# Kernel tuning notes

Hardware: AMD Instinct MI355X
Metric: run time of the kernel (lower is better)

## Reference

```python
import jax, jax.numpy as jnp
import numpy as np

B, E, FC_N = 8, 65536, 2500
CONVS = [5, 16, 32, 64, 64]
EPS = 1e-5


def setup_inputs() -> dict:
    key = jax.random.key(0)
    ks = iter(jax.random.split(key, 32))
    inp = {
        'x': jax.random.normal(next(ks), (B, 5, E), dtype=jnp.float32),
        'gemm': jax.random.randint(next(ks), (B, E, 4), 0, E, dtype=jnp.int32),
        'old_verts': jax.random.normal(next(ks), (B, 642, 3), dtype=jnp.float32),
    }
    for i in range(4):
        ci, co = CONVS[i], CONVS[i + 1]
        inp[f'w{i}'] = jax.random.normal(next(ks), (co, ci, 5), dtype=jnp.float32) * 0.02
        inp[f'b{i}'] = jnp.zeros((co,), dtype=jnp.float32)
        inp[f'g{i}'] = jnp.ones((co,), dtype=jnp.float32)
        inp[f'beta{i}'] = jnp.zeros((co,), dtype=jnp.float32)
    inp['dw1'] = jax.random.normal(next(ks), (FC_N, CONVS[-1]), dtype=jnp.float32) * 0.02
    inp['db1'] = jnp.zeros((FC_N,), dtype=jnp.float32)
    inp['dw2'] = jax.random.normal(next(ks), (642 * 3, FC_N), dtype=jnp.float32) * 0.02
    inp['db2'] = jnp.zeros((642 * 3,), dtype=jnp.float32)
    return inp


def mesh_conv(x, gemm, w, b):
    # x: (B,C,E); gemm: (B,E,4) -> neighbor features (B,C,E,4)
    nb = jax.vmap(lambda xb, gb: xb[:, gb])(x, gemm)
    # MeshCNN symmetric features: [self, a+c, b+d, |a-c|, |b-d|]
    f = jnp.stack([
        x,
        nb[..., 0] + nb[..., 2],
        nb[..., 1] + nb[..., 3],
        jnp.abs(nb[..., 0] - nb[..., 2]),
        jnp.abs(nb[..., 1] - nb[..., 3]),
    ], axis=-1)  # (B,C,E,5)
    return jnp.einsum('bcek,ock->boe', f, w) + b[None, :, None]


def bn_relu(x, g, beta):
    # BatchNorm2d training-mode math over (batch, spatial) per channel
    mean = jnp.mean(x, axis=(0, 2), keepdims=True)
    var = jnp.var(x, axis=(0, 2), keepdims=True)
    return jax.nn.relu((x - mean) * jax.lax.rsqrt(var + EPS) * g[None, :, None] + beta[None, :, None])


def reference(x, gemm, old_verts,
              w0, b0, g0, beta0, w1, b1, g1, beta1,
              w2, b2, g2, beta2, w3, b3, g3, beta3,
              dw1, db1, dw2, db2):
    h = x[:, :5]
    params = [(w0, b0, g0, beta0), (w1, b1, g1, beta1),
              (w2, b2, g2, beta2), (w3, b3, g3, beta3)]
    for w, b, g, beta in params:
        h = bn_relu(mesh_conv(h, gemm, w, b), g, beta)
    pooled = jnp.mean(h, axis=2)                 # AvgPool1d(n_edges) -> (B, C)
    h1 = jax.nn.relu(pooled @ dw1.T + db1)       # dropout = identity (eval)
    out = h1 @ dw2.T + db2
    return out.reshape(-1, 642, 3) + old_verts
```

## Files before the change

kernel.cpp:

```cpp
#include <hip/hip_runtime.h>

#define E_DIM 65536
#define BE_TOTAL 524288
#define EPS_BN 1e-5f
#define NB_STATS 256

typedef unsigned int uint;
typedef unsigned short ushort;
typedef unsigned char uchar;
typedef __attribute__((ext_vector_type(8))) short short8;
typedef __attribute__((ext_vector_type(4))) float floatx4;

#define PB_FP8 ((size_t)BE_TOTAL*16)

__device__ __forceinline__ float bflo(uint u){ return __uint_as_float(u << 16); }
__device__ __forceinline__ float bfhi(uint u){ return __uint_as_float(u & 0xffff0000u); }

__device__ __forceinline__ ushort pbf1(float a){
  uint ua = __float_as_uint(a);
  return (ushort)((ua + 0x7fffu + ((ua >> 16) & 1u)) >> 16);
}
__device__ __forceinline__ uint packbf(float a, float b){
  return (uint)pbf1(a) | ((uint)pbf1(b) << 16);
}
__device__ __forceinline__ void unpack8(uint4 v, float* x){
  x[0]=bflo(v.x); x[1]=bfhi(v.x); x[2]=bflo(v.y); x[3]=bfhi(v.y);
  x[4]=bflo(v.z); x[5]=bfhi(v.z); x[6]=bflo(v.w); x[7]=bfhi(v.w);
}
__device__ __forceinline__ uint4 pack8u(const float* z){
  uint4 v;
  v.x = packbf(z[0],z[1]); v.y = packbf(z[2],z[3]);
  v.z = packbf(z[4],z[5]); v.w = packbf(z[6],z[7]);
  return v;
}

__device__ __forceinline__ uint2 pack8f8(const float* z){
  int lo = __builtin_amdgcn_cvt_pk_fp8_f32(z[0], z[1], 0,  false);
  lo     = __builtin_amdgcn_cvt_pk_fp8_f32(z[2], z[3], lo, true);
  int hi = __builtin_amdgcn_cvt_pk_fp8_f32(z[4], z[5], 0,  false);
  hi     = __builtin_amdgcn_cvt_pk_fp8_f32(z[6], z[7], hi, true);
  uint2 r; r.x = (uint)lo; r.y = (uint)hi; return r;
}
__device__ __forceinline__ void dec8f8(uint2 w, float* x){
  x[0]=__builtin_amdgcn_cvt_f32_fp8((int)w.x,0);
  x[1]=__builtin_amdgcn_cvt_f32_fp8((int)w.x,1);
  x[2]=__builtin_amdgcn_cvt_f32_fp8((int)w.x,2);
  x[3]=__builtin_amdgcn_cvt_f32_fp8((int)w.x,3);
  x[4]=__builtin_amdgcn_cvt_f32_fp8((int)w.y,0);
  x[5]=__builtin_amdgcn_cvt_f32_fp8((int)w.y,1);
  x[6]=__builtin_amdgcn_cvt_f32_fp8((int)w.y,2);
  x[7]=__builtin_amdgcn_cvt_f32_fp8((int)w.y,3);
}
__device__ __forceinline__ uchar f8byte(float v){
  return (uchar)(__builtin_amdgcn_cvt_pk_fp8_f32(v, 0.f, 0, false) & 0xff);
}

template<int CI, int CO>
__global__ void wprep8(const float* __restrict__ w, uchar* __restrict__ img)
{
  constexpr int CHUNKS = CI/16;
  const int t = blockIdx.x*256 + threadIdx.x;
  if (t >= CHUNKS*3*CO*4) return;
  const int g  = t & 3;
  const int o  = (t >> 2) % CO;
  const int ck = (t >> 2) / CO;
  const int chunk = ck / 3;
  const int ks    = ck % 3;
  float z[8];
  #pragma unroll
  for (int j8=0;j8<8;j8++){
    const int j = g*8 + j8;
    const int ft = ks*2 + (j>>4);
    const int ci = chunk*16 + (j & 15);
    z[j8] = (ft < 5) ? w[((size_t)o*CI + ci)*5 + ft] * 64.f : 0.f;
  }
  const int t4 = (o&3) ^ ((o>>2)&3);
  *reinterpret_cast<uint2*>(img + ((size_t)(ck*CO + o))*32 + ((g^t4)<<3)) = pack8f8(z);
}

template<int CI, int CO, bool IN_FP8, bool OUT_BF16LIN>
__launch_bounds__(256, 4)
__global__ void mconv_mfma(const char* __restrict__ hin,
                           const int* __restrict__ gemm,
                           const char* __restrict__ wimg,
                           const float* __restrict__ bias, float bscale,
                           const float* __restrict__ ss, float pkf,
                           char* __restrict__ hout,
                           float* __restrict__ spart)
{
  constexpr int CHUNKS = CI/16;
  constexpr int NT = CO/16;
  constexpr int AB  = IN_FP8 ? 32 : 64;
  constexpr int FBY = 3*128*AB;
  constexpr int NBUF = (CHUNKS > 1) ? 2 : 1;
  constexpr int OBB = 128*CO*(OUT_BF16LIN?2:1);
  constexpr int SBY = 4*2*CO*4;
  constexpr int SMEM = (NBUF*FBY > OBB+SBY) ? NBUF*FBY : (OBB+SBY);
  constexpr size_t PIN = IN_FP8 ? PB_FP8 : (size_t)BE_TOTAL*32;
  constexpr int RB = IN_FP8 ? 16 : 32;
  __shared__ char smem[SMEM];
  char* FB = smem;

  const int tid = threadIdx.x;
  const int bid = blockIdx.x;
  const int b   = bid & 7;
  const int e0  = (bid >> 3) * 128;
  const size_t bbase = (size_t)b << 16;

  const int lane = tid & 63;
  const int wv   = tid >> 6;
  const int col  = lane & 15;
  const int kg   = lane >> 4;
  const int t4c  = (col & 3) ^ ((col >> 2) & 3);

  floatx4 acc[2][NT];
  #pragma unroll
  for (int n=0;n<NT;n++){
    const float bv = bias[n*16 + col] * bscale;
    #pragma unroll
    for (int mt=0;mt<2;mt++) acc[mt][n] = (floatx4){bv,bv,bv,bv};
  }

  const int el = tid >> 1;
  const int hh = tid & 1;
  const int t4e = (el&3) ^ ((el>>2)&3);
  uint off[5];
  {
    const size_t idx = bbase + (size_t)(e0 + el);
    const int4 g4 = *reinterpret_cast<const int4*>(gemm + idx*4);
    off[0] = (uint)(idx*RB + hh*(RB/2));
    off[1] = (uint)((bbase + (size_t)(uint)g4.x)*RB + hh*(RB/2));
    off[2] = (uint)((bbase + (size_t)(uint)g4.y)*RB + hh*(RB/2));
    off[3] = (uint)((bbase + (size_t)(uint)g4.z)*RB + hh*(RB/2));
    off[4] = (uint)((bbase + (size_t)(uint)g4.w)*RB + hh*(RB/2));
  }

  auto BUILD = [&](float (&v)[5][8], int chunk, char* FBb){
    const int cb = chunk*16 + hh*8;
    #pragma unroll
    for (int c=0;c<8;c++){
      const float sc = ss[cb+c], sh = ss[CI+cb+c];
      #pragma unroll
      for (int r=0;r<5;r++) v[r][c] = fmaxf(fmaf(v[r][c], sc, sh), 0.f);
    }
    float y[5][8];
    #pragma unroll
    for (int c=0;c<8;c++){
      y[0][c] = v[0][c];
      y[1][c] = v[1][c] + v[3][c];
      y[2][c] = v[2][c] + v[4][c];
      y[3][c] = fabsf(v[1][c] - v[3][c]);
      y[4][c] = fabsf(v[2][c] - v[4][c]);
    }
    if constexpr (IN_FP8){
      #pragma unroll
      for (int ks=0; ks<3; ks++){
        char* base = FBb + ks*(128*32) + el*32;
        *reinterpret_cast<uint2*>(base + (((0+hh)^t4e)<<3)) = pack8f8(y[2*ks]);
        if (ks < 2){
          *reinterpret_cast<uint2*>(base + (((2+hh)^t4e)<<3)) = pack8f8(y[2*ks+1]);
        } else {
          uint2 zz; zz.x=0u; zz.y=0u;
          *reinterpret_cast<uint2*>(base + (((2+hh)^t4e)<<3)) = zz;
        }
      }
    } else {
      #pragma unroll
      for (int ks=0; ks<3; ks++){
        char* base = FBb + ks*8192 + el*64;
        *reinterpret_cast<uint4*>(base + (((0+hh)^t4e)<<4)) = pack8u(y[2*ks]);
        if (ks < 2){
          *reinterpret_cast<uint4*>(base + (((2+hh)^t4e)<<4)) = pack8u(y[2*ks+1]);
        } else {
          const uint4 zz = {0,0,0,0};
          *reinterpret_cast<uint4*>(base + (((2+hh)^t4e)<<4)) = zz;
        }
      }
    }
  };

  auto MMA = [&](int chunk, const char* FBb){
    const char* WG = wimg + (size_t)chunk*(3*CO*AB);
    #pragma unroll
    for (int ks=0; ks<3; ks++){
      if constexpr (IN_FP8){
        long long bf[NT];
        #pragma unroll
        for (int n=0;n<NT;n++)
          bf[n] = *reinterpret_cast<const long long*>(WG + ks*(CO*32) + n*512 + col*32 + ((kg^t4c)<<3));
        #pragma unroll
        for (int mt=0;mt<2;mt++){
          const long long af = *reinterpret_cast<const long long*>(
              FBb + ks*(128*32) + (wv*32+mt*16+col)*32 + ((kg^t4c)<<3));
          #pragma unroll
          for (int n=0;n<NT;n++)
            acc[mt][n] = __builtin_amdgcn_mfma_f32_16x16x32_fp8_fp8(af, bf[n], acc[mt][n], 0, 0, 0);
        }
      } else {
        short8 bf[NT];
        #pragma unroll
        for (int n=0;n<NT;n++)
          bf[n] = *reinterpret_cast<const short8*>(WG + ks*(CO*64) + n*1024 + col*64 + ((kg^t4c)<<4));
        #pragma unroll
        for (int mt=0;mt<2;mt++){
          const short8 af = *reinterpret_cast<const short8*>(
              FBb + ks*8192 + (wv*32+mt*16+col)*64 + ((kg^t4c)<<4));
          #pragma unroll
          for (int n=0;n<NT;n++)
            acc[mt][n] = __builtin_amdgcn_mfma_f32_16x16x32_bf16(af, bf[n], acc[mt][n], 0, 0, 0);
        }
      }
    }
  };

  if constexpr (CHUNKS == 1){
    float v[5][8];
    uint2 q[5];
    #pragma unroll
    for (int r=0;r<5;r++) q[r] = *reinterpret_cast<const uint2*>(hin + off[r]);
    #pragma unroll
    for (int r=0;r<5;r++) dec8f8(q[r], v[r]);
    BUILD(v, 0, FB);
    __syncthreads();
    MMA(0, FB);
  } else {
    uint2 qs[2][5];
    #pragma unroll
    for (int r=0;r<5;r++) qs[0][r] = *reinterpret_cast<const uint2*>(hin + off[r]);
    {
      const char* hp1 = hin + PIN;
      #pragma unroll
      for (int r=0;r<5;r++) qs[1][r] = *reinterpret_cast<const uint2*>(hp1 + off[r]);
    }
    {
      float v[5][8];
      #pragma unroll
      for (int r=0;r<5;r++) dec8f8(qs[0][r], v[r]);
      BUILD(v, 0, FB);
    }
    __syncthreads();
    #pragma unroll
    for (int c=0; c<CHUNKS; ++c){
      if (c+2 < CHUNKS){
        const char* hp = hin + (size_t)(c+2)*PIN;
        #pragma unroll
        for (int r=0;r<5;r++) qs[c&1][r] = *reinterpret_cast<const uint2*>(hp + off[r]);
      }
      MMA(c, FB + (c&1)*FBY);
      if (c+1 < CHUNKS){
        float v[5][8];
        #pragma unroll
        for (int r=0;r<5;r++) dec8f8(qs[(c+1)&1][r], v[r]);
        BUILD(v, c+1, FB + ((c+1)&1)*FBY);
        __syncthreads();
      }
    }
  }

  float sred[2*NT];
  #pragma unroll
  for (int n=0;n<NT;n++){
    float s = 0.f, q2 = 0.f;
    #pragma unroll
    for (int mt=0;mt<2;mt++){
      #pragma unroll
      for (int r=0;r<4;r++){ const float vv = acc[mt][n][r]; s += vv; q2 = fmaf(vv,vv,q2); }
    }
    s  += __shfl_xor(s,16,64);  s  += __shfl_xor(s,32,64);
    q2 += __shfl_xor(q2,16,64); q2 += __shfl_xor(q2,32,64);
    sred[n] = s; sred[NT+n] = q2;
  }

  __syncthreads();
  float* SB = reinterpret_cast<float*>(smem + OBB);
  if constexpr (OUT_BF16LIN){
    ushort* OB = reinterpret_cast<ushort*>(smem);
    #pragma unroll
    for (int mt=0; mt<2; mt++){
      const int er = wv*32 + mt*16 + 4*kg;
      #pragma unroll
      for (int n=0;n<NT;n++){
        #pragma unroll
        for (int r=0;r<4;r++)
          OB[(er+r)*CO + n*16 + col] = pbf1(acc[mt][n][r]);
      }
    }
  } else {
    uchar* OB = reinterpret_cast<uchar*>(smem);
    #pragma unroll
    for (int mt=0; mt<2; mt++){
      const int er = wv*32 + mt*16 + 4*kg;
      #pragma unroll
      for (int n=0;n<NT;n++){
        #pragma unroll
        for (int r=0;r<4;r++)
          OB[(er+r)*CO + n*16 + col] = f8byte(acc[mt][n][r] * pkf);
      }
    }
  }
  if (kg == 0){
    #pragma unroll
    for (int n=0;n<NT;n++){
      SB[wv*2*CO + n*16 + col]      = sred[n];
      SB[wv*2*CO + CO + n*16 + col] = sred[NT+n];
    }
  }
  __syncthreads();
  if constexpr (OUT_BF16LIN){
    const uint4* src = reinterpret_cast<const uint4*>(smem);
    uint4* dst = reinterpret_cast<uint4*>(hout + (bbase + (size_t)e0)*CO*2);
    constexpr int NV = 128*CO/8;
    for (int i=tid; i<NV; i+=256) dst[i] = src[i];
  } else {
    constexpr int NV = 128*CO/16;
    for (int i=tid; i<NV; i+=256){
      const int pl  = i >> 7;
      const int elx = i & 127;
      const uint4 vv = *reinterpret_cast<const uint4*>(smem + elx*CO + pl*16);
      *reinterpret_cast<uint4*>(hout + (size_t)pl*PB_FP8 + (bbase + (size_t)(e0+elx))*16) = vv;
    }
  }
  if (tid < 2*CO){
    spart[(size_t)bid*2*CO + tid] =
      SB[tid] + SB[2*CO + tid] + SB[4*CO + tid] + SB[6*CO + tid];
  }
}

__launch_bounds__(256)
__global__ void conv0_kernel(const ushort* __restrict__ hin,
                             const int* __restrict__ gemm,
                             const float* __restrict__ w,
                             const float* __restrict__ bias,
                             char* __restrict__ hout)
{
  const int bid = blockIdx.x;
  const int swz = (bid & 7) * 256 + (bid >> 3);
  const int idx = swz * 256 + threadIdx.x;
  const int b = idx >> 16;
  const int4 g4 = *reinterpret_cast<const int4*>(gemm + (size_t)idx * 4);
  const size_t bbase = (size_t)b << 16;
  float xc[8], n0[8], n1[8], n2[8], n3[8];
  unpack8(*reinterpret_cast<const uint4*>(hin + (size_t)idx*8), xc);
  unpack8(*reinterpret_cast<const uint4*>(hin + (bbase + (size_t)(uint)g4.x)*8), n0);
  unpack8(*reinterpret_cast<const uint4*>(hin + (bbase + (size_t)(uint)g4.y)*8), n1);
  unpack8(*reinterpret_cast<const uint4*>(hin + (bbase + (size_t)(uint)g4.z)*8), n2);
  unpack8(*reinterpret_cast<const uint4*>(hin + (bbase + (size_t)(uint)g4.w)*8), n3);
  float f1[5], f2[5], f3[5], f4[5];
  #pragma unroll
  for (int c=0;c<5;c++){
    f1[c] = n0[c] + n2[c];
    f2[c] = n1[c] + n3[c];
    f3[c] = fabsf(n0[c] - n2[c]);
    f4[c] = fabsf(n1[c] - n3[c]);
  }
  float acc[16];
  #pragma unroll
  for (int o=0;o<16;o++){
    const float* wp = w + (size_t)o*25;
    float a = bias[o];
    #pragma unroll
    for (int c=0;c<5;c++){
      a = fmaf(xc[c], wp[c*5+0], a);
      a = fmaf(f1[c], wp[c*5+1], a);
      a = fmaf(f2[c], wp[c*5+2], a);
      a = fmaf(f3[c], wp[c*5+3], a);
      a = fmaf(f4[c], wp[c*5+4], a);
    }
    acc[o] = a * 16.f;
  }
  const uint2 lo = pack8f8(acc);
  const uint2 hi = pack8f8(acc + 8);
  uint4 v; v.x = lo.x; v.y = lo.y; v.z = hi.x; v.w = hi.y;
  *reinterpret_cast<uint4*>(hout + (size_t)idx * 16) = v;
}

__launch_bounds__(256)
__global__ void stats8_16(const char* __restrict__ h, float* __restrict__ part)
{
  const int tid = threadIdx.x;
  const int cg  = tid & 1;
  const int row = tid >> 1;
  float s[8], q[8];
  #pragma unroll
  for (int i=0;i<8;i++){ s[i]=0.f; q[i]=0.f; }
  for (long idx = (long)blockIdx.x*128 + row; idx < BE_TOTAL; idx += (long)gridDim.x*128){
    uint2 v = *reinterpret_cast<const uint2*>(h + idx*16 + cg*8);
    float x[8]; dec8f8(v, x);
    #pragma unroll
    for (int i=0;i<8;i++){ s[i]+=x[i]; q[i]+=x[i]*x[i]; }
  }
  __shared__ float lds[256*16];
  #pragma unroll
  for (int i=0;i<8;i++){ lds[tid*16+i]=s[i]; lds[tid*16+8+i]=q[i]; }
  __syncthreads();
  if (tid < 32){
    const int st = tid / 16;
    const int c  = tid % 16;
    const int cgg = c >> 3, ci = c & 7;
    float t = 0.f;
    for (int r=0;r<128;r++) t += lds[(r*2+cgg)*16 + st*8 + ci];
    part[(size_t)blockIdx.x*32 + tid] = t;
  }
}

template<int CO>
__launch_bounds__(256)
__global__ void merge_stats(const float* __restrict__ in, float* __restrict__ out)
{
  const int t = threadIdx.x;
  if (t >= 2*CO) return;
  const int j = blockIdx.x;
  float s = 0.f;
  #pragma unroll 4
  for (int r = 0; r < 32; r++) s += in[((size_t)(j*32 + r))*(2*CO) + t];
  out[(size_t)j*(2*CO) + t] = s;
}

template<int CO>
__launch_bounds__(256)
__global__ void finalize_stats(const float* __restrict__ part, int nblk,
                               const float* __restrict__ g, const float* __restrict__ beta,
                               float invSa, float invSt, float* __restrict__ ss)
{
  constexpr int Q = 256 / CO;
  const int t = threadIdx.x;
  const int c = t % CO;
  const int qq = t / CO;
  float s = 0.f, sq = 0.f;
  for (int b = qq; b < nblk; b += Q){
    s  += part[(size_t)b*2*CO + c];
    sq += part[(size_t)b*2*CO + CO + c];
  }
  __shared__ float lsum[256], lsq[256];
  lsum[t] = s; lsq[t] = sq;
  __syncthreads();
  if (t < CO){
    float ts = 0.f, tq = 0.f;
    #pragma unroll
    for (int r = 0; r < Q; r++){ ts += lsum[r*CO + t]; tq += lsq[r*CO + t]; }
    const float inv = 1.f / (float)BE_TOTAL;
    const float mean = ts * inv * invSa;
    const float var  = tq * inv * invSa * invSa - mean*mean;
    const float scale = g[t] * rsqrtf(var + EPS_BN);
    ss[t]      = scale * invSt;
    ss[CO + t] = beta[t] - mean * scale;
  }
}

__launch_bounds__(256)
__global__ void pool_kernel(const char* __restrict__ h3, const float* __restrict__ ss,
                            float* __restrict__ part)
{
  const int tid = threadIdx.x;
  const int cg  = tid % 8;
  const int row = tid / 8;
  const int b   = blockIdx.x >> 6;
  const int blk = blockIdx.x & 63;
  float sc[8], sh[8];
  #pragma unroll
  for (int i=0;i<8;i++){ sc[i]=ss[cg*8+i]; sh[i]=ss[64+cg*8+i]; }
  float s[8];
  #pragma unroll
  for (int i=0;i<8;i++) s[i]=0.f;
  const char* hp = h3 + (size_t)(cg>>1)*PB_FP8 + (cg&1)*8;
  for (int e = blk*32 + row; e < E_DIM; e += 64*32){
    size_t idx = ((size_t)b << 16) + e;
    uint2 v = *reinterpret_cast<const uint2*>(hp + idx*16);
    float x[8]; dec8f8(v, x);
    #pragma unroll
    for (int i=0;i<8;i++) s[i] += fmaxf(fmaf(x[i], sc[i], sh[i]), 0.f);
  }
  __shared__ float lds[256*8];
  #pragma unroll
  for (int i=0;i<8;i++) lds[tid*8+i]=s[i];
  __syncthreads();
  if (tid < 64){
    const int c = tid, cgg = c >> 3, ci = c & 7;
    float t = 0.f;
    for (int r=0;r<32;r++) t += lds[(r*8+cgg)*8 + ci];
    part[((size_t)b*64 + blk)*64 + c] = t;
  }
}

__global__ void finalize_pool(const float* __restrict__ part, float* __restrict__ pooled)
{
  const int t = threadIdx.x;
  const int b = t >> 6, c = t & 63;
  float s = 0.f;
  for (int blk=0;blk<64;blk++) s += part[((size_t)b*64 + blk)*64 + c];
  pooled[t] = s * (1.f / (float)E_DIM);
}

__global__ void fc1_kernel(const float* __restrict__ pooled, const float* __restrict__ dw1,
                           const float* __restrict__ db1, float* __restrict__ h1t)
{
  const int n = blockIdx.x*blockDim.x + threadIdx.x;
  if (n >= 2500) return;
  float acc[8];
  const float bias = db1[n];
  #pragma unroll
  for (int b=0;b<8;b++) acc[b]=bias;
  const float* wr = dw1 + (size_t)n*64;
  #pragma unroll
  for (int c=0;c<64;c++){
    float wv = wr[c];
    #pragma unroll
    for (int b=0;b<8;b++) acc[b] = fmaf(wv, pooled[b*64+c], acc[b]);
  }
  #pragma unroll
  for (int b=0;b<8;b++) h1t[(size_t)n*8 + b] = fmaxf(acc[b], 0.f);
}

__launch_bounds__(256)
__global__ void fc2_kernel(const float* __restrict__ h1t, const float* __restrict__ dw2,
                           const float* __restrict__ db2, const float* __restrict__ oldv,
                           float* __restrict__ out)
{
  const int wv   = threadIdx.x >> 6;
  const int lane = threadIdx.x & 63;
  const int m = blockIdx.x*4 + wv;
  if (m >= 1926) return;
  const float4* wr = reinterpret_cast<const float4*>(dw2 + (size_t)m*2500);
  float acc[8];
  #pragma unroll
  for (int b=0;b<8;b++) acc[b]=0.f;
  for (int j = lane; j < 625; j += 64){
    const float4 w4 = wr[j];
    const float4* hp = reinterpret_cast<const float4*>(h1t + (size_t)j*32);
    const float4 h0a = hp[0], h0b = hp[1];
    const float4 h1a = hp[2], h1b = hp[3];
    const float4 h2a = hp[4], h2b = hp[5];
    const float4 h3a = hp[6], h3b = hp[7];
    acc[0] = fmaf(w4.x, h0a.x, fmaf(w4.y, h1a.x, fmaf(w4.z, h2a.x, fmaf(w4.w, h3a.x, acc[0]))));
    acc[1] = fmaf(w4.x, h0a.y, fmaf(w4.y, h1a.y, fmaf(w4.z, h2a.y, fmaf(w4.w, h3a.y, acc[1]))));
    acc[2] = fmaf(w4.x, h0a.z, fmaf(w4.y, h1a.z, fmaf(w4.z, h2a.z, fmaf(w4.w, h3a.z, acc[2]))));
    acc[3] = fmaf(w4.x, h0a.w, fmaf(w4.y, h1a.w, fmaf(w4.z, h2a.w, fmaf(w4.w, h3a.w, acc[3]))));
    acc[4] = fmaf(w4.x, h0b.x, fmaf(w4.y, h1b.x, fmaf(w4.z, h2b.x, fmaf(w4.w, h3b.x, acc[4]))));
    acc[5] = fmaf(w4.x, h0b.y, fmaf(w4.y, h1b.y, fmaf(w4.z, h2b.y, fmaf(w4.w, h3b.y, acc[5]))));
    acc[6] = fmaf(w4.x, h0b.z, fmaf(w4.y, h1b.z, fmaf(w4.z, h2b.z, fmaf(w4.w, h3b.z, acc[6]))));
    acc[7] = fmaf(w4.x, h0b.w, fmaf(w4.y, h1b.w, fmaf(w4.z, h2b.w, fmaf(w4.w, h3b.w, acc[7]))));
  }
  #pragma unroll
  for (int s=1; s<64; s<<=1){
    #pragma unroll
    for (int b=0;b<8;b++) acc[b] += __shfl_xor(acc[b], s, 64);
  }
  if (lane == 0){
    const float bm = db2[m];
    #pragma unroll
    for (int b=0;b<8;b++){
      const int t = b*1926 + m;
      out[t] = acc[b] + bm + oldv[t];
    }
  }
}

__launch_bounds__(256)
__global__ void transpose_x(const float* __restrict__ x, ushort* __restrict__ xt)
{
  const int idx = blockIdx.x*256 + threadIdx.x;
  const int b = idx >> 16, e = idx & 65535;
  const float* xb = x + (size_t)b*5*E_DIM + e;
  uint4 v;
  v.x = packbf(xb[0],               xb[(size_t)E_DIM]);
  v.y = packbf(xb[2*(size_t)E_DIM], xb[3*(size_t)E_DIM]);
  v.z = packbf(xb[4*(size_t)E_DIM], 0.f);
  v.w = 0u;
  *reinterpret_cast<uint4*>(xt + (size_t)idx*8) = v;
}

extern "C" void kernel_launch(void* const* d_in, const int* in_sizes, int n_in,
                              void* d_out, int out_size, void* d_ws, size_t ws_size,
                              hipStream_t stream)
{
  const float* x    = (const float*)d_in[0];
  const int*   gm   = (const int*)d_in[1];
  const float* oldv = (const float*)d_in[2];
  const float* w0 = (const float*)d_in[3],  *b0 = (const float*)d_in[4];
  const float* g0 = (const float*)d_in[5],  *be0= (const float*)d_in[6];
  const float* w1 = (const float*)d_in[7],  *b1 = (const float*)d_in[8];
  const float* g1 = (const float*)d_in[9],  *be1= (const float*)d_in[10];
  const float* w2 = (const float*)d_in[11], *b2 = (const float*)d_in[12];
  const float* g2 = (const float*)d_in[13], *be2= (const float*)d_in[14];
  const float* w3 = (const float*)d_in[15], *b3 = (const float*)d_in[16];
  const float* g3 = (const float*)d_in[17], *be3= (const float*)d_in[18];
  const float* dw1 = (const float*)d_in[19], *db1 = (const float*)d_in[20];
  const float* dw2 = (const float*)d_in[21], *db2 = (const float*)d_in[22];

  char* ws = (char*)d_ws;
  size_t off = 0;
  auto alloc = [&](size_t n){ size_t o = off; off += (n + 255) & ~(size_t)255; return o; };
  ushort* xt = (ushort*)(ws + alloc((size_t)BE_TOTAL*8*2));
  char*   h0 = (char*)  (ws + alloc((size_t)BE_TOTAL*16));
  char*   h1 = (char*)  (ws + alloc((size_t)BE_TOTAL*32));
  char*   h2 = (char*)  (ws + alloc((size_t)BE_TOTAL*64));
  char*   h3 = (char*)  (ws + alloc((size_t)BE_TOTAL*64));
  float* part   = (float*)(ws + alloc((size_t)NB_STATS*128*4));
  float* spart  = (float*)(ws + alloc((size_t)4096*128*4));
  float* mpart  = (float*)(ws + alloc((size_t)128*128*4));
  float* ss0    = (float*)(ws + alloc(512));
  float* ss1    = (float*)(ws + alloc(512));
  float* ss2    = (float*)(ws + alloc(512));
  float* ss3    = (float*)(ws + alloc(512));
  float* ppart  = (float*)(ws + alloc((size_t)8*64*64*4));
  float* pooled = (float*)(ws + alloc(512*4));
  float* h1fc   = (float*)(ws + alloc(20000*4));
  uchar*  w1i   = (uchar*) (ws + alloc((size_t)3*32*32));
  uchar*  w2i   = (uchar*) (ws + alloc((size_t)6*64*32));
  uchar*  w3i   = (uchar*) (ws + alloc((size_t)12*64*32));
  (void)ws_size; (void)in_sizes; (void)n_in; (void)out_size;

  const int CB = BE_TOTAL/256;
  const int MB = BE_TOTAL/128;

  transpose_x<<<CB,256,0,stream>>>(x, xt);
  wprep8<16,32><<<2,256,0,stream>>>(w1, w1i);
  wprep8<32,64><<<6,256,0,stream>>>(w2, w2i);
  wprep8<64,64><<<12,256,0,stream>>>(w3, w3i);

  conv0_kernel<<<CB,256,0,stream>>>(xt, gm, w0, b0, h0);
  stats8_16<<<NB_STATS,256,0,stream>>>(h0, part);
  finalize_stats<16><<<1,256,0,stream>>>(part, NB_STATS, g0, be0, 1.f/16.f, 1.f/16.f, ss0);

  mconv_mfma<16,32,true,false><<<MB,256,0,stream>>>(
      h0, gm, (const char*)w1i, b1, 64.f, ss0, 0.25f, h1, spart);
  merge_stats<32><<<128,256,0,stream>>>(spart, mpart);
  finalize_stats<32><<<1,256,0,stream>>>(mpart, 128, g1, be1, 1.f/64.f, 1.f/16.f, ss1);

  mconv_mfma<32,64,true,false><<<MB,256,0,stream>>>(
      h1, gm, (const char*)w2i, b2, 64.f, ss1, 0.25f, h2, spart);
  merge_stats<64><<<128,256,0,stream>>>(spart, mpart);
  finalize_stats<64><<<1,256,0,stream>>>(mpart, 128, g2, be2, 1.f/64.f, 1.f/16.f, ss2);

  mconv_mfma<64,64,true,false><<<MB,256,0,stream>>>(
      h2, gm, (const char*)w3i, b3, 64.f, ss2, 0.25f, h3, spart);
  merge_stats<64><<<128,256,0,stream>>>(spart, mpart);
  finalize_stats<64><<<1,256,0,stream>>>(mpart, 128, g3, be3, 1.f/64.f, 1.f/16.f, ss3);

  pool_kernel<<<512,256,0,stream>>>(h3, ss3, ppart);
  finalize_pool<<<1,512,0,stream>>>(ppart, pooled);
  fc1_kernel<<<10,256,0,stream>>>(pooled, dw1, db1, h1fc);
  fc2_kernel<<<482,256,0,stream>>>(h1fc, dw2, db2, oldv, (float*)d_out);
}
```

Before: 246.4 us.

## Pre-normalize activations and fold symmetric sums into weights for MFMA conv

Adds a separate norm_k pass that applies BN scale/shift and ReLU and rewrites fp8 activations before each mesh conv. The conv kernel no longer decodes and normalizes gathered neighbors. It writes the raw neighbor fp8 bytes straight into LDS and folds the a+c and b+d sums into the weights by duplicating weight columns, so K grows from 3 to 4 steps per chunk. Only the abs-difference features are still computed, by decoding, subtracting, packing and clearing the sign bit. This removes per-gather ALU work but adds an extra full read/write pass over every activation tensor, more MFMA work and more weight data.

```diff
diff --git a/kernel.cpp b/kernel.cpp
--- a/kernel.cpp
+++ b/kernel.cpp
@@ -8,7 +8,6 @@
 typedef unsigned int uint;
 typedef unsigned short ushort;
 typedef unsigned char uchar;
-typedef __attribute__((ext_vector_type(8))) short short8;
 typedef __attribute__((ext_vector_type(4))) float floatx4;
 
 #define PB_FP8 ((size_t)BE_TOTAL*16)
@@ -26,12 +25,6 @@
 __device__ __forceinline__ void unpack8(uint4 v, float* x){
   x[0]=bflo(v.x); x[1]=bfhi(v.x); x[2]=bflo(v.y); x[3]=bfhi(v.y);
   x[4]=bflo(v.z); x[5]=bfhi(v.z); x[6]=bflo(v.w); x[7]=bfhi(v.w);
-}
-__device__ __forceinline__ uint4 pack8u(const float* z){
-  uint4 v;
-  v.x = packbf(z[0],z[1]); v.y = packbf(z[2],z[3]);
-  v.z = packbf(z[4],z[5]); v.w = packbf(z[6],z[7]);
-  return v;
 }
 
 __device__ __forceinline__ uint2 pack8f8(const float* z){
@@ -60,44 +53,43 @@
 {
   constexpr int CHUNKS = CI/16;
   const int t = blockIdx.x*256 + threadIdx.x;
-  if (t >= CHUNKS*3*CO*4) return;
-  const int g  = t & 3;
-  const int o  = (t >> 2) % CO;
-  const int ck = (t >> 2) / CO;
-  const int chunk = ck / 3;
-  const int ks    = ck % 3;
+  if (t >= CHUNKS*4*CO*4) return;
+  const int sub8 = t & 3;
+  const int o    = (t >> 2) % CO;
+  const int ck   = (t >> 2) / CO;
+  const int chunk = ck / 4;
+  const int ks    = ck % 4;
+  const int ftmap[8] = {0,1,2,1,2,3,4,-1};
   float z[8];
   #pragma unroll
-  for (int j8=0;j8<8;j8++){
-    const int j = g*8 + j8;
-    const int ft = ks*2 + (j>>4);
+  for (int i=0;i<8;i++){
+    const int j = ks*32 + sub8*8 + i;
+    const int g = j >> 4;
     const int ci = chunk*16 + (j & 15);
-    z[j8] = (ft < 5) ? w[((size_t)o*CI + ci)*5 + ft] * 64.f : 0.f;
+    const int ft = ftmap[g];
+    z[i] = (ft >= 0) ? w[((size_t)o*CI + ci)*5 + ft] * 64.f : 0.f;
   }
   const int t4 = (o&3) ^ ((o>>2)&3);
-  *reinterpret_cast<uint2*>(img + ((size_t)(ck*CO + o))*32 + ((g^t4)<<3)) = pack8f8(z);
-}
-
-template<int CI, int CO, bool IN_FP8, bool OUT_BF16LIN>
+  *reinterpret_cast<uint2*>(img + ((size_t)(ck*CO + o))*32 + ((sub8^t4)<<3)) = pack8f8(z);
+}
+
+template<int CI, int CO>
 __launch_bounds__(256, 4)
-__global__ void mconv_mfma(const char* __restrict__ hin,
+__global__ void mconv_mfma(const char* __restrict__ nh,
                            const int* __restrict__ gemm,
                            const char* __restrict__ wimg,
                            const float* __restrict__ bias, float bscale,
-                           const float* __restrict__ ss, float pkf,
+                           float pkf,
                            char* __restrict__ hout,
                            float* __restrict__ spart)
 {
   constexpr int CHUNKS = CI/16;
   constexpr int NT = CO/16;
-  constexpr int AB  = IN_FP8 ? 32 : 64;
-  constexpr int FBY = 3*128*AB;
+  constexpr int FBY = 4*128*32;
   constexpr int NBUF = (CHUNKS > 1) ? 2 : 1;
-  constexpr int OBB = 128*CO*(OUT_BF16LIN?2:1);
+  constexpr int OBB = 128*CO;
   constexpr int SBY = 4*2*CO*4;
   constexpr int SMEM = (NBUF*FBY > OBB+SBY) ? NBUF*FBY : (OBB+SBY);
-  constexpr size_t PIN = IN_FP8 ? PB_FP8 : (size_t)BE_TOTAL*32;
-  constexpr int RB = IN_FP8 ? 16 : 32;
   __shared__ char smem[SMEM];
   char* FB = smem;
 
@@ -128,130 +120,89 @@
   {
     const size_t idx = bbase + (size_t)(e0 + el);
     const int4 g4 = *reinterpret_cast<const int4*>(gemm + idx*4);
-    off[0] = (uint)(idx*RB + hh*(RB/2));
-    off[1] = (uint)((bbase + (size_t)(uint)g4.x)*RB + hh*(RB/2));
-    off[2] = (uint)((bbase + (size_t)(uint)g4.y)*RB + hh*(RB/2));
-    off[3] = (uint)((bbase + (size_t)(uint)g4.z)*RB + hh*(RB/2));
-    off[4] = (uint)((bbase + (size_t)(uint)g4.w)*RB + hh*(RB/2));
-  }
-
-  auto BUILD = [&](float (&v)[5][8], int chunk, char* FBb){
-    const int cb = chunk*16 + hh*8;
-    #pragma unroll
-    for (int c=0;c<8;c++){
-      const float sc = ss[cb+c], sh = ss[CI+cb+c];
+    off[0] = (uint)(idx*16 + hh*8);
+    off[1] = (uint)((bbase + (size_t)(uint)g4.x)*16 + hh*8);
+    off[2] = (uint)((bbase + (size_t)(uint)g4.y)*16 + hh*8);
+    off[3] = (uint)((bbase + (size_t)(uint)g4.z)*16 + hh*8);
+    off[4] = (uint)((bbase + (size_t)(uint)g4.w)*16 + hh*8);
+  }
+
+  auto BUILD = [&](uint2 (&q)[5], char* FBb){
+    #pragma unroll
+    for (int g=0; g<5; g++){
+      char* base = FBb + (g>>1)*4096 + el*32;
+      *reinterpret_cast<uint2*>(base + ((((g&1)*2+hh)^t4e)<<3)) = q[g];
+    }
+    float va[8], vb[8], d[8];
+    dec8f8(q[1], va); dec8f8(q[3], vb);
+    #pragma unroll
+    for (int i=0;i<8;i++) d[i] = va[i] - vb[i];
+    {
+      uint2 u = pack8f8(d);
+      u.x &= 0x7f7f7f7fu; u.y &= 0x7f7f7f7fu;
+      *reinterpret_cast<uint2*>(FBb + 2*4096 + el*32 + (((2+hh)^t4e)<<3)) = u;
+    }
+    dec8f8(q[2], va); dec8f8(q[4], vb);
+    #pragma unroll
+    for (int i=0;i<8;i++) d[i] = va[i] - vb[i];
+    {
+      uint2 u = pack8f8(d);
+      u.x &= 0x7f7f7f7fu; u.y &= 0x7f7f7f7fu;
+      *reinterpret_cast<uint2*>(FBb + 3*4096 + el*32 + (((0+hh)^t4e)<<3)) = u;
+    }
+    {
+      uint2 zz; zz.x = 0u; zz.y = 0u;
+      *reinterpret_cast<uint2*>(FBb + 3*4096 + el*32 + (((2+hh)^t4e)<<3)) = zz;
+    }
+  };
+
+  auto MMA = [&](int chunk, const char* FBb){
+    const char* WG = wimg + (size_t)chunk*(4*CO*32);
+    #pragma unroll
+    for (int ks=0; ks<4; ks++){
+      long long bf[NT];
       #pragma unroll
-      for (int r=0;r<5;r++) v[r][c] = fmaxf(fmaf(v[r][c], sc, sh), 0.f);
-    }
-    float y[5][8];
-    #pragma unroll
-    for (int c=0;c<8;c++){
-      y[0][c] = v[0][c];
-      y[1][c] = v[1][c] + v[3][c];
-      y[2][c] = v[2][c] + v[4][c];
-      y[3][c] = fabsf(v[1][c] - v[3][c]);
-      y[4][c] = fabsf(v[2][c] - v[4][c]);
-    }
-    if constexpr (IN_FP8){
+      for (int n=0;n<NT;n++)
+        bf[n] = *reinterpret_cast<const long long*>(WG + ks*(CO*32) + n*512 + col*32 + ((kg^t4c)<<3));
       #pragma unroll
-      for (int ks=0; ks<3; ks++){
-        char* base = FBb + ks*(128*32) + el*32;
-        *reinterpret_cast<uint2*>(base + (((0+hh)^t4e)<<3)) = pack8f8(y[2*ks]);
-        if (ks < 2){
-          *reinterpret_cast<uint2*>(base + (((2+hh)^t4e)<<3)) = pack8f8(y[2*ks+1]);
-        } else {
-          uint2 zz; zz.x=0u; zz.y=0u;
-          *reinterpret_cast<uint2*>(base + (((2+hh)^t4e)<<3)) = zz;
-        }
-      }
-    } else {
-      #pragma unroll
-      for (int ks=0; ks<3; ks++){
-        char* base = FBb + ks*8192 + el*64;
-        *reinterpret_cast<uint4*>(base + (((0+hh)^t4e)<<4)) = pack8u(y[2*ks]);
-        if (ks < 2){
-          *reinterpret_cast<uint4*>(base + (((2+hh)^t4e)<<4)) = pack8u(y[2*ks+1]);
-        } else {
-          const uint4 zz = {0,0,0,0};
-          *reinterpret_cast<uint4*>(base + (((2+hh)^t4e)<<4)) = zz;
-        }
-      }
-    }
-  };
-
-  auto MMA = [&](int chunk, const char* FBb){
-    const char* WG = wimg + (size_t)chunk*(3*CO*AB);
-    #pragma unroll
-    for (int ks=0; ks<3; ks++){
-      if constexpr (IN_FP8){
-        long long bf[NT];
+      for (int mt=0;mt<2;mt++){
+        const long long af = *reinterpret_cast<const long long*>(
+            FBb + ks*4096 + (wv*32+mt*16+col)*32 + ((kg^t4c)<<3));
         #pragma unroll
         for (int n=0;n<NT;n++)
-          bf[n] = *reinterpret_cast<const long long*>(WG + ks*(CO*32) + n*512 + col*32 + ((kg^t4c)<<3));
-        #pragma unroll
-        for (int mt=0;mt<2;mt++){
-          const long long af = *reinterpret_cast<const long long*>(
-              FBb + ks*(128*32) + (wv*32+mt*16+col)*32 + ((kg^t4c)<<3));
-          #pragma unroll
-          for (int n=0;n<NT;n++)
-            acc[mt][n] = __builtin_amdgcn_mfma_f32_16x16x32_fp8_fp8(af, bf[n], acc[mt][n], 0, 0, 0);
-        }
-      } else {
-        short8 bf[NT];
-        #pragma unroll
-        for (int n=0;n<NT;n++)
-          bf[n] = *reinterpret_cast<const short8*>(WG + ks*(CO*64) + n*1024 + col*64 + ((kg^t4c)<<4));
-        #pragma unroll
-        for (int mt=0;mt<2;mt++){
-          const short8 af = *reinterpret_cast<const short8*>(
-              FBb + ks*8192 + (wv*32+mt*16+col)*64 + ((kg^t4c)<<4));
-          #pragma unroll
-          for (int n=0;n<NT;n++)
-            acc[mt][n] = __builtin_amdgcn_mfma_f32_16x16x32_bf16(af, bf[n], acc[mt][n], 0, 0, 0);
-        }
+          acc[mt][n] = __builtin_amdgcn_mfma_f32_16x16x32_fp8_fp8(af, bf[n], acc[mt][n], 0, 0, 0);
       }
     }
   };
 
   if constexpr (CHUNKS == 1){
-    float v[5][8];
     uint2 q[5];
     #pragma unroll
-    for (int r=0;r<5;r++) q[r] = *reinterpret_cast<const uint2*>(hin + off[r]);
-    #pragma unroll
-    for (int r=0;r<5;r++) dec8f8(q[r], v[r]);
-    BUILD(v, 0, FB);
+    for (int r=0;r<5;r++) q[r] = *reinterpret_cast<const uint2*>(nh + off[r]);
+    BUILD(q, FB);
     __syncthreads();
     MMA(0, FB);
   } else {
     uint2 qs[2][5];
     #pragma unroll
-    for (int r=0;r<5;r++) qs[0][r] = *reinterpret_cast<const uint2*>(hin + off[r]);
+    for (int r=0;r<5;r++) qs[0][r] = *reinterpret_cast<const uint2*>(nh + off[r]);
     {
-      const char* hp1 = hin + PIN;
+      const char* hp1 = nh + PB_FP8;
       #pragma unroll
       for (int r=0;r<5;r++) qs[1][r] = *reinterpret_cast<const uint2*>(hp1 + off[r]);
     }
-    {
-      float v[5][8];
-      #pragma unroll
-      for (int r=0;r<5;r++) dec8f8(qs[0][r], v[r]);
-      BUILD(v, 0, FB);
-    }
+    BUILD(qs[0], FB);
     __syncthreads();
     #pragma unroll
     for (int c=0; c<CHUNKS; ++c){
       if (c+2 < CHUNKS){
-        const char* hp = hin + (size_t)(c+2)*PIN;
+        const char* hp = nh + (size_t)(c+2)*PB_FP8;
         #pragma unroll
         for (int r=0;r<5;r++) qs[c&1][r] = *reinterpret_cast<const uint2*>(hp + off[r]);
       }
       MMA(c, FB + (c&1)*FBY);
       if (c+1 < CHUNKS){
-        float v[5][8];
-        #pragma unroll
-        for (int r=0;r<5;r++) dec8f8(qs[(c+1)&1][r], v[r]);
-        BUILD(v, c+1, FB + ((c+1)&1)*FBY);
+        BUILD(qs[(c+1)&1], FB + ((c+1)&1)*FBY);
         __syncthreads();
       }
     }
@@ -273,19 +224,7 @@
 
   __syncthreads();
   float* SB = reinterpret_cast<float*>(smem + OBB);
-  if constexpr (OUT_BF16LIN){
-    ushort* OB = reinterpret_cast<ushort*>(smem);
-    #pragma unroll
-    for (int mt=0; mt<2; mt++){
-      const int er = wv*32 + mt*16 + 4*kg;
-      #pragma unroll
-      for (int n=0;n<NT;n++){
-        #pragma unroll
-        for (int r=0;r<4;r++)
-          OB[(er+r)*CO + n*16 + col] = pbf1(acc[mt][n][r]);
-      }
-    }
-  } else {
+  {
     uchar* OB = reinterpret_cast<uchar*>(smem);
     #pragma unroll
     for (int mt=0; mt<2; mt++){
@@ -306,12 +245,7 @@
     }
   }
   __syncthreads();
-  if constexpr (OUT_BF16LIN){
-    const uint4* src = reinterpret_cast<const uint4*>(smem);
-    uint4* dst = reinterpret_cast<uint4*>(hout + (bbase + (size_t)e0)*CO*2);
-    constexpr int NV = 128*CO/8;
-    for (int i=tid; i<NV; i+=256) dst[i] = src[i];
-  } else {
+  {
     constexpr int NV = 128*CO/16;
     for (int i=tid; i<NV; i+=256){
       const int pl  = i >> 7;
@@ -324,6 +258,35 @@
     spart[(size_t)bid*2*CO + tid] =
       SB[tid] + SB[2*CO + tid] + SB[4*CO + tid] + SB[6*CO + tid];
   }
+}
+
+template<int CI>
+__launch_bounds__(256)
+__global__ void norm_k(const char* __restrict__ h, const float* __restrict__ ss,
+                       char* __restrict__ nh)
+{
+  constexpr int SP = BE_TOTAL/256;
+  const int plane = blockIdx.x / SP;
+  const int sp    = blockIdx.x % SP;
+  const size_t idx = (size_t)sp*256 + threadIdx.x;
+  const int cb = plane*16;
+  const char* src = h  + (size_t)plane*PB_FP8 + idx*16;
+  char*       dst = nh + (size_t)plane*PB_FP8 + idx*16;
+  uint4 v = *reinterpret_cast<const uint4*>(src);
+  float x[16];
+  uint2 lo; lo.x = v.x; lo.y = v.y;
+  uint2 hi; hi.x = v.z; hi.y = v.w;
+  dec8f8(lo, x); dec8f8(hi, x+8);
+  float y[16];
+  #pragma unroll
+  for (int i=0;i<16;i++){
+    const float sc = ss[cb+i]*16.f, sh = ss[CI+cb+i]*16.f;
+    y[i] = fmaxf(fmaf(x[i], sc, sh), 0.f);
+  }
+  const uint2 a = pack8f8(y);
+  const uint2 c = pack8f8(y+8);
+  uint4 o; o.x = a.x; o.y = a.y; o.z = c.x; o.w = c.y;
+  *reinterpret_cast<uint4*>(dst) = o;
 }
 
 __launch_bounds__(256)
@@ -595,6 +558,9 @@
   char*   h1 = (char*)  (ws + alloc((size_t)BE_TOTAL*32));
   char*   h2 = (char*)  (ws + alloc((size_t)BE_TOTAL*64));
   char*   h3 = (char*)  (ws + alloc((size_t)BE_TOTAL*64));
+  char*   nh0= (char*)  (ws + alloc((size_t)BE_TOTAL*16));
+  char*   nh1= (char*)  (ws + alloc((size_t)BE_TOTAL*32));
+  char*   nh2= (char*)  (ws + alloc((size_t)BE_TOTAL*64));
   float* part   = (float*)(ws + alloc((size_t)NB_STATS*128*4));
   float* spart  = (float*)(ws + alloc((size_t)4096*128*4));
   float* mpart  = (float*)(ws + alloc((size_t)128*128*4));
@@ -605,37 +571,38 @@
   float* ppart  = (float*)(ws + alloc((size_t)8*64*64*4));
   float* pooled = (float*)(ws + alloc(512*4));
   float* h1fc   = (float*)(ws + alloc(20000*4));
-  uchar*  w1i   = (uchar*) (ws + alloc((size_t)3*32*32));
-  uchar*  w2i   = (uchar*) (ws + alloc((size_t)6*64*32));
-  uchar*  w3i   = (uchar*) (ws + alloc((size_t)12*64*32));
+  uchar*  w1i   = (uchar*) (ws + alloc((size_t)4*32*32));
+  uchar*  w2i   = (uchar*) (ws + alloc((size_t)8*64*32));
+  uchar*  w3i   = (uchar*) (ws + alloc((size_t)16*64*32));
   (void)ws_size; (void)in_sizes; (void)n_in; (void)out_size;
 
   const int CB = BE_TOTAL/256;
   const int MB = BE_TOTAL/128;
+  const int SP = BE_TOTAL/256;
 
   transpose_x<<<CB,256,0,stream>>>(x, xt);
   wprep8<16,32><<<2,256,0,stream>>>(w1, w1i);
-  wprep8<32,64><<<6,256,0,stream>>>(w2, w2i);
-  wprep8<64,64><<<12,256,0,stream>>>(w3, w3i);
+  wprep8<32,64><<<8,256,0,stream>>>(w2, w2i);
+  wprep8<64,64><<<16,256,0,stream>>>(w3, w3i);
 
   conv0_kernel<<<CB,256,0,stream>>>(xt, gm, w0, b0, h0);
   stats8_16<<<NB_STATS,256,0,stream>>>(h0, part);
   finalize_stats<16><<<1,256,0,stream>>>(part, NB_STATS, g0, be0, 1.f/16.f, 1.f/16.f, ss0);
-
-  mconv_mfma<16,32,true,false><<<MB,256,0,stream>>>(
-      h0, gm, (const char*)w1i, b1, 64.f, ss0, 0.25f, h1, spart);
+  norm_k<16><<<1*SP,256,0,stream>>>(h0, ss0, nh0);
+
+  mconv_mfma<16,32><<<MB,256,0,stream>>>(nh0, gm, (const char*)w1i, b1, 1024.f, 1.f/64.f, h1, spart);
   merge_stats<32><<<128,256,0,stream>>>(spart, mpart);
-  finalize_stats<32><<<1,256,0,stream>>>(mpart, 128, g1, be1, 1.f/64.f, 1.f/16.f, ss1);
-
-  mconv_mfma<32,64,true,false><<<MB,256,0,stream>>>(
-      h1, gm, (const char*)w2i, b2, 64.f, ss1, 0.25f, h2, spart);
+  finalize_stats<32><<<1,256,0,stream>>>(mpart, 128, g1, be1, 1.f/1024.f, 1.f/16.f, ss1);
+  norm_k<32><<<2*SP,256,0,stream>>>(h1, ss1, nh1);
+
+  mconv_mfma<32,64><<<MB,256,0,stream>>>(nh1, gm, (const char*)w2i, b2, 1024.f, 1.f/64.f, h2, spart);
   merge_stats<64><<<128,256,0,stream>>>(spart, mpart);
-  finalize_stats<64><<<1,256,0,stream>>>(mpart, 128, g2, be2, 1.f/64.f, 1.f/16.f, ss2);
-
-  mconv_mfma<64,64,true,false><<<MB,256,0,stream>>>(
-      h2, gm, (const char*)w3i, b3, 64.f, ss2, 0.25f, h3, spart);
+  finalize_stats<64><<<1,256,0,stream>>>(mpart, 128, g2, be2, 1.f/1024.f, 1.f/16.f, ss2);
+  norm_k<64><<<4*SP,256,0,stream>>>(h2, ss2, nh2);
+
+  mconv_mfma<64,64><<<MB,256,0,stream>>>(nh2, gm, (const char*)w3i, b3, 1024.f, 1.f/64.f, h3, spart);
   merge_stats<64><<<128,256,0,stream>>>(spart, mpart);
-  finalize_stats<64><<<1,256,0,stream>>>(mpart, 128, g3, be3, 1.f/64.f, 1.f/16.f, ss3);
+  finalize_stats<64><<<1,256,0,stream>>>(mpart, 128, g3, be3, 1.f/1024.f, 1.f/16.f, ss3);
 
   pool_kernel<<<512,256,0,stream>>>(h3, ss3, ppart);
   finalize_pool<<<1,512,0,stream>>>(ppart, pooled);
```

Measured after the change: 265.0 us. +7.6%, slower.
